# Kernel optimization log

Measured on AMD Instinct MI355X. Metric: run time of the kernel, lower is better.

Reference implementation:

```python
import jax, jax.numpy as jnp
import numpy as np

EPS = 1e-8  # torch F.cosine_similarity default eps


def setup_inputs() -> dict:
    key = jax.random.key(0)
    k1, k2, k3 = jax.random.split(key, 3)
    B, D, C = 65536, 512, 10000
    embeddings = jax.random.normal(k1, (B, D), dtype=jnp.float32)
    labels = jax.random.randint(k2, (B,), 0, C, dtype=jnp.int64)
    prototypes = jax.random.normal(k3, (C, D), dtype=jnp.float32)
    return {"embeddings": embeddings, "labels": labels, "prototypes": prototypes}


def reference(embeddings, labels, prototypes):
    # Batched gather of per-sample prototypes: [B, D]
    protos = prototypes[labels]
    # Cosine similarity per sample (torch eps semantics: clamp norm at eps)
    e_norm = jnp.maximum(jnp.linalg.norm(embeddings, axis=-1), EPS)
    p_norm = jnp.maximum(jnp.linalg.norm(protos, axis=-1), EPS)
    cos = jnp.sum(embeddings * protos, axis=-1) / (e_norm * p_norm)
    return 1.0 - jnp.mean(cos)
```

## Files before the change

kernel.cpp:

```cpp
#include <hip/hip_runtime.h>
#include <math.h>

#define COS_EPS 1e-8f

__global__ __launch_bounds__(256) void assignment_loss_kernel(
    const float* __restrict__ emb,
    const int*   __restrict__ labels,
    const float* __restrict__ protos,
    float*       __restrict__ acc,
    int B, int D)
{
    const int lane           = threadIdx.x & 63;
    const int wave_in_block  = threadIdx.x >> 6;
    const int waves_per_blk  = blockDim.x >> 6;
    const int global_wave    = blockIdx.x * waves_per_blk + wave_in_block;
    const int n_waves        = gridDim.x * waves_per_blk;
    const int nchunks        = D >> 8;

    float local = 0.0f;

    for (int s = global_wave; s < B; s += n_waves) {
        const int lbl = labels[s];
        const float4* __restrict__ e =
            (const float4*)(emb + (size_t)s * (size_t)D);
        const float4* __restrict__ p =
            (const float4*)(protos + (size_t)lbl * (size_t)D);

        float dot = 0.0f, esq = 0.0f, psq = 0.0f;
        #pragma unroll
        for (int c = 0; c < 2; ++c) {
            if (c < nchunks) {
                float4 ev = e[c * 64 + lane];
                float4 pv = p[c * 64 + lane];
                dot = fmaf(ev.x, pv.x, fmaf(ev.y, pv.y, fmaf(ev.z, pv.z, fmaf(ev.w, pv.w, dot))));
                esq = fmaf(ev.x, ev.x, fmaf(ev.y, ev.y, fmaf(ev.z, ev.z, fmaf(ev.w, ev.w, esq))));
                psq = fmaf(pv.x, pv.x, fmaf(pv.y, pv.y, fmaf(pv.z, pv.z, fmaf(pv.w, pv.w, psq))));
            }
        }
        for (int c = 2; c < nchunks; ++c) {
            float4 ev = e[c * 64 + lane];
            float4 pv = p[c * 64 + lane];
            dot = fmaf(ev.x, pv.x, fmaf(ev.y, pv.y, fmaf(ev.z, pv.z, fmaf(ev.w, pv.w, dot))));
            esq = fmaf(ev.x, ev.x, fmaf(ev.y, ev.y, fmaf(ev.z, ev.z, fmaf(ev.w, ev.w, esq))));
            psq = fmaf(pv.x, pv.x, fmaf(pv.y, pv.y, fmaf(pv.z, pv.z, fmaf(pv.w, pv.w, psq))));
        }

        #pragma unroll
        for (int off = 32; off > 0; off >>= 1) {
            dot += __shfl_xor(dot, off, 64);
            esq += __shfl_xor(esq, off, 64);
            psq += __shfl_xor(psq, off, 64);
        }

        if (lane == 0) {
            float en = fmaxf(sqrtf(esq), COS_EPS);
            float pn = fmaxf(sqrtf(psq), COS_EPS);
            local += dot / (en * pn);
        }
    }

    __shared__ float smem[8];
    if (lane == 0) smem[wave_in_block] = local;
    __syncthreads();
    if (threadIdx.x == 0) {
        float bs = 0.0f;
        for (int w = 0; w < waves_per_blk; ++w) bs += smem[w];
        atomicAdd(acc, bs);
    }
}

__global__ void assignment_loss_finalize(const float* __restrict__ acc,
                                         float* __restrict__ out,
                                         float invB)
{
    out[0] = 1.0f - acc[0] * invB;
}

extern "C" void kernel_launch(void* const* d_in, const int* in_sizes, int n_in,
                              void* d_out, int out_size, void* d_ws, size_t ws_size,
                              hipStream_t stream) {
    const float* emb    = (const float*)d_in[0];
    const int*   labels = (const int*)  d_in[1];
    const float* protos = (const float*)d_in[2];
    float*       out    = (float*)d_out;
    float*       acc    = (float*)d_ws;

    const int B = in_sizes[1];
    const int D = in_sizes[0] / B;

    hipMemsetAsync(acc, 0, sizeof(float), stream);

    const int block = 256;
    const int grid  = 1024;
    assignment_loss_kernel<<<grid, block, 0, stream>>>(emb, labels, protos, acc, B, D);
    assignment_loss_finalize<<<1, 1, 0, stream>>>(acc, out, 1.0f / (float)B);
}
```

Measured before the change: 215.2 us.

## Process two samples per wave with nontemporal loads and fuse finalize via ticket

Each wave now handles two samples per iteration, which doubles the loads in flight to hide gather latency. Embedding reads use nontemporal loads so streaming data does not evict cached prototypes. The separate finalize kernel is replaced by a last-block-done ticket reduction over per-block partials. The grid is doubled to 2048 blocks. This adds register pressure and a threadfence/atomic handshake at the end of the kernel.

```diff
diff --git a/kernel.cpp b/kernel.cpp
--- a/kernel.cpp
+++ b/kernel.cpp
@@ -3,77 +3,120 @@
 
 #define COS_EPS 1e-8f
 
+typedef float vfloat4 __attribute__((ext_vector_type(4)));
+
 __global__ __launch_bounds__(256) void assignment_loss_kernel(
     const float* __restrict__ emb,
     const int*   __restrict__ labels,
     const float* __restrict__ protos,
-    float*       __restrict__ acc,
-    int B, int D)
+    float*        __restrict__ partials,
+    unsigned int* __restrict__ ticket,
+    float*        __restrict__ out,
+    int B, int D, float invB)
 {
-    const int lane           = threadIdx.x & 63;
-    const int wave_in_block  = threadIdx.x >> 6;
-    const int waves_per_blk  = blockDim.x >> 6;
-    const int global_wave    = blockIdx.x * waves_per_blk + wave_in_block;
-    const int n_waves        = gridDim.x * waves_per_blk;
-    const int nchunks        = D >> 8;
+    const int lane          = threadIdx.x & 63;
+    const int wave_in_block = threadIdx.x >> 6;
+    const int waves_per_blk = blockDim.x >> 6;
+    const int global_wave   = blockIdx.x * waves_per_blk + wave_in_block;
+    const int n_waves       = gridDim.x * waves_per_blk;
+    const int nchunks       = D >> 8;
 
     float local = 0.0f;
 
-    for (int s = global_wave; s < B; s += n_waves) {
-        const int lbl = labels[s];
-        const float4* __restrict__ e =
-            (const float4*)(emb + (size_t)s * (size_t)D);
-        const float4* __restrict__ p =
-            (const float4*)(protos + (size_t)lbl * (size_t)D);
+    for (int s0 = global_wave; s0 < B; s0 += 2 * n_waves) {
+        const int s1    = s0 + n_waves;
+        const bool has1 = (s1 < B);
 
-        float dot = 0.0f, esq = 0.0f, psq = 0.0f;
+        const int l0 = labels[s0];
+        const int l1 = has1 ? labels[s1] : 0;
+
+        const vfloat4* __restrict__ e0 = (const vfloat4*)(emb    + (size_t)s0 * (size_t)D);
+        const vfloat4* __restrict__ p0 = (const vfloat4*)(protos + (size_t)l0 * (size_t)D);
+        const vfloat4* __restrict__ e1 = (const vfloat4*)(emb    + (size_t)(has1 ? s1 : s0) * (size_t)D);
+        const vfloat4* __restrict__ p1 = (const vfloat4*)(protos + (size_t)l1 * (size_t)D);
+
+        float dot0 = 0.f, esq0 = 0.f, psq0 = 0.f;
+        float dot1 = 0.f, esq1 = 0.f, psq1 = 0.f;
+
         #pragma unroll
         for (int c = 0; c < 2; ++c) {
             if (c < nchunks) {
-                float4 ev = e[c * 64 + lane];
-                float4 pv = p[c * 64 + lane];
-                dot = fmaf(ev.x, pv.x, fmaf(ev.y, pv.y, fmaf(ev.z, pv.z, fmaf(ev.w, pv.w, dot))));
-                esq = fmaf(ev.x, ev.x, fmaf(ev.y, ev.y, fmaf(ev.z, ev.z, fmaf(ev.w, ev.w, esq))));
-                psq = fmaf(pv.x, pv.x, fmaf(pv.y, pv.y, fmaf(pv.z, pv.z, fmaf(pv.w, pv.w, psq))));
+                vfloat4 ev0 = __builtin_nontemporal_load(&e0[c * 64 + lane]);
+                vfloat4 pv0 = p0[c * 64 + lane];
+                vfloat4 ev1 = __builtin_nontemporal_load(&e1[c * 64 + lane]);
+                vfloat4 pv1 = p1[c * 64 + lane];
+
+                dot0 = fmaf(ev0.x, pv0.x, fmaf(ev0.y, pv0.y, fmaf(ev0.z, pv0.z, fmaf(ev0.w, pv0.w, dot0))));
+                esq0 = fmaf(ev0.x, ev0.x, fmaf(ev0.y, ev0.y, fmaf(ev0.z, ev0.z, fmaf(ev0.w, ev0.w, esq0))));
+                psq0 = fmaf(pv0.x, pv0.x, fmaf(pv0.y, pv0.y, fmaf(pv0.z, pv0.z, fmaf(pv0.w, pv0.w, psq0))));
+                dot1 = fmaf(ev1.x, pv1.x, fmaf(ev1.y, pv1.y, fmaf(ev1.z, pv1.z, fmaf(ev1.w, pv1.w, dot1))));
+                esq1 = fmaf(ev1.x, ev1.x, fmaf(ev1.y, ev1.y, fmaf(ev1.z, ev1.z, fmaf(ev1.w, ev1.w, esq1))));
+                psq1 = fmaf(pv1.x, pv1.x, fmaf(pv1.y, pv1.y, fmaf(pv1.z, pv1.z, fmaf(pv1.w, pv1.w, psq1))));
             }
         }
         for (int c = 2; c < nchunks; ++c) {
-            float4 ev = e[c * 64 + lane];
-            float4 pv = p[c * 64 + lane];
-            dot = fmaf(ev.x, pv.x, fmaf(ev.y, pv.y, fmaf(ev.z, pv.z, fmaf(ev.w, pv.w, dot))));
-            esq = fmaf(ev.x, ev.x, fmaf(ev.y, ev.y, fmaf(ev.z, ev.z, fmaf(ev.w, ev.w, esq))));
-            psq = fmaf(pv.x, pv.x, fmaf(pv.y, pv.y, fmaf(pv.z, pv.z, fmaf(pv.w, pv.w, psq))));
+            vfloat4 ev0 = __builtin_nontemporal_load(&e0[c * 64 + lane]);
+            vfloat4 pv0 = p0[c * 64 + lane];
+            vfloat4 ev1 = __builtin_nontemporal_load(&e1[c * 64 + lane]);
+            vfloat4 pv1 = p1[c * 64 + lane];
+            dot0 = fmaf(ev0.x, pv0.x, fmaf(ev0.y, pv0.y, fmaf(ev0.z, pv0.z, fmaf(ev0.w, pv0.w, dot0))));
+            esq0 = fmaf(ev0.x, ev0.x, fmaf(ev0.y, ev0.y, fmaf(ev0.z, ev0.z, fmaf(ev0.w, ev0.w, esq0))));
+            psq0 = fmaf(pv0.x, pv0.x, fmaf(pv0.y, pv0.y, fmaf(pv0.z, pv0.z, fmaf(pv0.w, pv0.w, psq0))));
+            dot1 = fmaf(ev1.x, pv1.x, fmaf(ev1.y, pv1.y, fmaf(ev1.z, pv1.z, fmaf(ev1.w, pv1.w, dot1))));
+            esq1 = fmaf(ev1.x, ev1.x, fmaf(ev1.y, ev1.y, fmaf(ev1.z, ev1.z, fmaf(ev1.w, ev1.w, esq1))));
+            psq1 = fmaf(pv1.x, pv1.x, fmaf(pv1.y, pv1.y, fmaf(pv1.z, pv1.z, fmaf(pv1.w, pv1.w, psq1))));
         }
 
         #pragma unroll
         for (int off = 32; off > 0; off >>= 1) {
-            dot += __shfl_xor(dot, off, 64);
-            esq += __shfl_xor(esq, off, 64);
-            psq += __shfl_xor(psq, off, 64);
+            dot0 += __shfl_xor(dot0, off, 64);
+            esq0 += __shfl_xor(esq0, off, 64);
+            psq0 += __shfl_xor(psq0, off, 64);
+            dot1 += __shfl_xor(dot1, off, 64);
+            esq1 += __shfl_xor(esq1, off, 64);
+            psq1 += __shfl_xor(psq1, off, 64);
         }
 
         if (lane == 0) {
-            float en = fmaxf(sqrtf(esq), COS_EPS);
-            float pn = fmaxf(sqrtf(psq), COS_EPS);
-            local += dot / (en * pn);
+            float en0 = fmaxf(sqrtf(esq0), COS_EPS);
+            float pn0 = fmaxf(sqrtf(psq0), COS_EPS);
+            local += dot0 / (en0 * pn0);
+            if (has1) {
+                float en1 = fmaxf(sqrtf(esq1), COS_EPS);
+                float pn1 = fmaxf(sqrtf(psq1), COS_EPS);
+                local += dot1 / (en1 * pn1);
+            }
         }
     }
 
     __shared__ float smem[8];
+    __shared__ bool  am_last;
     if (lane == 0) smem[wave_in_block] = local;
     __syncthreads();
     if (threadIdx.x == 0) {
         float bs = 0.0f;
         for (int w = 0; w < waves_per_blk; ++w) bs += smem[w];
-        atomicAdd(acc, bs);
+        partials[blockIdx.x] = bs;
+        __threadfence();
+        unsigned t = atomicAdd(ticket, 1u);
+        am_last = (t == (unsigned)gridDim.x - 1u);
     }
-}
+    __syncthreads();
 
-__global__ void assignment_loss_finalize(const float* __restrict__ acc,
-                                         float* __restrict__ out,
-                                         float invB)
-{
-    out[0] = 1.0f - acc[0] * invB;
+    if (am_last) {
+        __threadfence();
+        float s = 0.0f;
+        for (int i = threadIdx.x; i < gridDim.x; i += blockDim.x) s += partials[i];
+        #pragma unroll
+        for (int off = 32; off > 0; off >>= 1) s += __shfl_xor(s, off, 64);
+        if (lane == 0) smem[wave_in_block] = s;
+        __syncthreads();
+        if (threadIdx.x == 0) {
+            float total = 0.0f;
+            for (int w = 0; w < waves_per_blk; ++w) total += smem[w];
+            out[0] = 1.0f - total * invB;
+        }
+    }
 }
 
 extern "C" void kernel_launch(void* const* d_in, const int* in_sizes, int n_in,
@@ -83,15 +126,17 @@
     const int*   labels = (const int*)  d_in[1];
     const float* protos = (const float*)d_in[2];
     float*       out    = (float*)d_out;
-    float*       acc    = (float*)d_ws;
+
+    unsigned int* ticket   = (unsigned int*)d_ws;
+    float*        partials = (float*)((char*)d_ws + 256);
 
     const int B = in_sizes[1];
     const int D = in_sizes[0] / B;
 
-    hipMemsetAsync(acc, 0, sizeof(float), stream);
+    hipMemsetAsync(ticket, 0, sizeof(unsigned int), stream);
 
     const int block = 256;
-    const int grid  = 1024;
-    assignment_loss_kernel<<<grid, block, 0, stream>>>(emb, labels, protos, acc, B, D);
-    assignment_loss_finalize<<<1, 1, 0, stream>>>(acc, out, 1.0f / (float)B);
+    const int grid  = 2048;
+    assignment_loss_kernel<<<grid, block, 0, stream>>>(
+        emb, labels, protos, partials, ticket, out, B, D, 1.0f / (float)B);
 }
```

Measured after the change: 298.3 us. +38.6%, slower.

## Precompute inverse row norms and defer wave reductions in weighted dot pass

Applied to the files above, without the earlier changes.

Splits the loss into two kernels. The first computes inverse L2 norms for every embedding row and every prototype row into workspace. The second computes only per-sample dot products scaled by the precomputed inverse norms, processing four samples per wave iteration for memory-level parallelism. It reduces across lanes once at the end instead of running three shuffle reductions per sample. The cost is a second full read of the embeddings plus one extra kernel launch, in exchange for much less per-sample shuffle and divide latency.

```diff
diff --git a/kernel.cpp b/kernel.cpp
--- a/kernel.cpp
+++ b/kernel.cpp
@@ -3,68 +3,123 @@
 
 #define COS_EPS 1e-8f
 
-__global__ __launch_bounds__(256) void assignment_loss_kernel(
+typedef float vfloat4 __attribute__((ext_vector_type(4)));
+
+__device__ __forceinline__ float dot4(vfloat4 a, vfloat4 b) {
+    return fmaf(a.x, b.x, fmaf(a.y, b.y, fmaf(a.z, b.z, a.w * b.w)));
+}
+
+__global__ __launch_bounds__(256) void row_inv_norm_kernel(
+    const float* __restrict__ emb,
+    const float* __restrict__ protos,
+    float* __restrict__ inv_en,
+    float* __restrict__ inv_pn,
+    int B, int C, int D)
+{
+    const int lane = threadIdx.x & 63;
+    const int gw   = (blockIdx.x * blockDim.x + threadIdx.x) >> 6;
+    const int nw   = (gridDim.x * blockDim.x) >> 6;
+    const int nchunks = D >> 8;
+    const int R = B + C;
+
+    for (int r = gw; r < R; r += nw) {
+        const float* row = (r < B) ? (emb + (size_t)r * (size_t)D)
+                                   : (protos + (size_t)(r - B) * (size_t)D);
+        const vfloat4* v = (const vfloat4*)row;
+        float ssq = 0.0f;
+        if (nchunks == 2) {
+            vfloat4 a = v[lane];
+            vfloat4 b = v[64 + lane];
+            ssq = dot4(a, a) + dot4(b, b);
+        } else {
+            for (int c = 0; c < nchunks; ++c) {
+                vfloat4 a = v[c * 64 + lane];
+                ssq += dot4(a, a);
+            }
+        }
+        #pragma unroll
+        for (int off = 32; off > 0; off >>= 1) ssq += __shfl_xor(ssq, off, 64);
+        if (lane == 0) {
+            float inv = 1.0f / fmaxf(sqrtf(ssq), COS_EPS);
+            if (r < B) inv_en[r] = inv; else inv_pn[r - B] = inv;
+        }
+    }
+}
+
+__global__ __launch_bounds__(256) void weighted_dot_kernel(
     const float* __restrict__ emb,
     const int*   __restrict__ labels,
     const float* __restrict__ protos,
+    const float* __restrict__ inv_en,
+    const float* __restrict__ inv_pn,
     float*       __restrict__ acc,
     int B, int D)
 {
-    const int lane           = threadIdx.x & 63;
-    const int wave_in_block  = threadIdx.x >> 6;
-    const int waves_per_blk  = blockDim.x >> 6;
-    const int global_wave    = blockIdx.x * waves_per_blk + wave_in_block;
-    const int n_waves        = gridDim.x * waves_per_blk;
-    const int nchunks        = D >> 8;
+    const int lane = threadIdx.x & 63;
+    const int wib  = threadIdx.x >> 6;
+    const int wpb  = blockDim.x >> 6;
+    const int gw   = blockIdx.x * wpb + wib;
+    const int nw   = gridDim.x * wpb;
+    const int nchunks = D >> 8;
 
     float local = 0.0f;
 
-    for (int s = global_wave; s < B; s += n_waves) {
-        const int lbl = labels[s];
-        const float4* __restrict__ e =
-            (const float4*)(emb + (size_t)s * (size_t)D);
-        const float4* __restrict__ p =
-            (const float4*)(protos + (size_t)lbl * (size_t)D);
+    if (nchunks == 2 && (B % (4 * nw)) == 0) {
+        for (int s = gw; s < B; s += 4 * nw) {
+            const int s0 = s, s1 = s + nw, s2 = s + 2 * nw, s3 = s + 3 * nw;
+            const int l0 = labels[s0], l1 = labels[s1], l2 = labels[s2], l3 = labels[s3];
 
-        float dot = 0.0f, esq = 0.0f, psq = 0.0f;
-        #pragma unroll
-        for (int c = 0; c < 2; ++c) {
-            if (c < nchunks) {
-                float4 ev = e[c * 64 + lane];
-                float4 pv = p[c * 64 + lane];
-                dot = fmaf(ev.x, pv.x, fmaf(ev.y, pv.y, fmaf(ev.z, pv.z, fmaf(ev.w, pv.w, dot))));
-                esq = fmaf(ev.x, ev.x, fmaf(ev.y, ev.y, fmaf(ev.z, ev.z, fmaf(ev.w, ev.w, esq))));
-                psq = fmaf(pv.x, pv.x, fmaf(pv.y, pv.y, fmaf(pv.z, pv.z, fmaf(pv.w, pv.w, psq))));
-            }
+            const vfloat4* e0 = (const vfloat4*)(emb    + (size_t)s0 * (size_t)D);
+            const vfloat4* e1 = (const vfloat4*)(emb    + (size_t)s1 * (size_t)D);
+            const vfloat4* e2 = (const vfloat4*)(emb    + (size_t)s2 * (size_t)D);
+            const vfloat4* e3 = (const vfloat4*)(emb    + (size_t)s3 * (size_t)D);
+            const vfloat4* p0 = (const vfloat4*)(protos + (size_t)l0 * (size_t)D);
+            const vfloat4* p1 = (const vfloat4*)(protos + (size_t)l1 * (size_t)D);
+            const vfloat4* p2 = (const vfloat4*)(protos + (size_t)l2 * (size_t)D);
+            const vfloat4* p3 = (const vfloat4*)(protos + (size_t)l3 * (size_t)D);
+
+            vfloat4 ea0 = e0[lane],      eb0 = e0[64 + lane];
+            vfloat4 ea1 = e1[lane],      eb1 = e1[64 + lane];
+            vfloat4 ea2 = e2[lane],      eb2 = e2[64 + lane];
+            vfloat4 ea3 = e3[lane],      eb3 = e3[64 + lane];
+            vfloat4 pa0 = p0[lane],      pb0 = p0[64 + lane];
+            vfloat4 pa1 = p1[lane],      pb1 = p1[64 + lane];
+            vfloat4 pa2 = p2[lane],      pb2 = p2[64 + lane];
+            vfloat4 pa3 = p3[lane],      pb3 = p3[64 + lane];
+
+            const float w0 = inv_en[s0] * inv_pn[l0];
+            const float w1 = inv_en[s1] * inv_pn[l1];
+            const float w2 = inv_en[s2] * inv_pn[l2];
+            const float w3 = inv_en[s3] * inv_pn[l3];
+
+            const float pd0 = dot4(ea0, pa0) + dot4(eb0, pb0);
+            const float pd1 = dot4(ea1, pa1) + dot4(eb1, pb1);
+            const float pd2 = dot4(ea2, pa2) + dot4(eb2, pb2);
+            const float pd3 = dot4(ea3, pa3) + dot4(eb3, pb3);
+
+            local = fmaf(pd0, w0, fmaf(pd1, w1, fmaf(pd2, w2, fmaf(pd3, w3, local))));
         }
-        for (int c = 2; c < nchunks; ++c) {
-            float4 ev = e[c * 64 + lane];
-            float4 pv = p[c * 64 + lane];
-            dot = fmaf(ev.x, pv.x, fmaf(ev.y, pv.y, fmaf(ev.z, pv.z, fmaf(ev.w, pv.w, dot))));
-            esq = fmaf(ev.x, ev.x, fmaf(ev.y, ev.y, fmaf(ev.z, ev.z, fmaf(ev.w, ev.w, esq))));
-            psq = fmaf(pv.x, pv.x, fmaf(pv.y, pv.y, fmaf(pv.z, pv.z, fmaf(pv.w, pv.w, psq))));
-        }
-
-        #pragma unroll
-        for (int off = 32; off > 0; off >>= 1) {
-            dot += __shfl_xor(dot, off, 64);
-            esq += __shfl_xor(esq, off, 64);
-            psq += __shfl_xor(psq, off, 64);
-        }
-
-        if (lane == 0) {
-            float en = fmaxf(sqrtf(esq), COS_EPS);
-            float pn = fmaxf(sqrtf(psq), COS_EPS);
-            local += dot / (en * pn);
+    } else {
+        for (int s = gw; s < B; s += nw) {
+            const int l = labels[s];
+            const vfloat4* e = (const vfloat4*)(emb    + (size_t)s * (size_t)D);
+            const vfloat4* p = (const vfloat4*)(protos + (size_t)l * (size_t)D);
+            float pd = 0.0f;
+            for (int c = 0; c < nchunks; ++c)
+                pd += dot4(e[c * 64 + lane], p[c * 64 + lane]);
+            local = fmaf(pd, inv_en[s] * inv_pn[l], local);
         }
     }
 
+    #pragma unroll
+    for (int off = 32; off > 0; off >>= 1) local += __shfl_xor(local, off, 64);
+
     __shared__ float smem[8];
-    if (lane == 0) smem[wave_in_block] = local;
+    if (lane == 0) smem[wib] = local;
     __syncthreads();
     if (threadIdx.x == 0) {
         float bs = 0.0f;
-        for (int w = 0; w < waves_per_blk; ++w) bs += smem[w];
+        for (int w = 0; w < wpb; ++w) bs += smem[w];
         atomicAdd(acc, bs);
     }
 }
@@ -83,15 +138,18 @@
     const int*   labels = (const int*)  d_in[1];
     const float* protos = (const float*)d_in[2];
     float*       out    = (float*)d_out;
-    float*       acc    = (float*)d_ws;
 
     const int B = in_sizes[1];
     const int D = in_sizes[0] / B;
+    const int C = in_sizes[2] / D;
+
+    float* acc    = (float*)d_ws;
+    float* inv_en = (float*)((char*)d_ws + 256);
+    float* inv_pn = inv_en + B;
 
     hipMemsetAsync(acc, 0, sizeof(float), stream);
 
-    const int block = 256;
-    const int grid  = 1024;
-    assignment_loss_kernel<<<grid, block, 0, stream>>>(emb, labels, protos, acc, B, D);
+    row_inv_norm_kernel<<<2048, 256, 0, stream>>>(emb, protos, inv_en, inv_pn, B, C, D);
+    weighted_dot_kernel<<<1024, 256, 0, stream>>>(emb, labels, protos, inv_en, inv_pn, acc, B, D);
     assignment_loss_finalize<<<1, 1, 0, stream>>>(acc, out, 1.0f / (float)B);
 }
```

After: 245.1 us. 1.14x slower.

## Process four samples per wave with 16-lane groups and prefetch labels

Applied to the files above, without the earlier changes.

Specializes the D=512 case so each wave handles four samples at once, with 16 lanes per sample each issuing eight float4 loads for the embedding and the prototype up front. The next sample's label is prefetched one iteration ahead, and the cross-lane reduction is shortened to four shuffle steps within each 16-lane group. This is meant to raise memory-level parallelism and hide the dependent label-then-prototype gather latency in a bandwidth-bound kernel. It costs more registers per thread, and it falls back to the old path when D or B do not fit the assumptions.

```diff
diff --git a/kernel.cpp b/kernel.cpp
--- a/kernel.cpp
+++ b/kernel.cpp
@@ -2,6 +2,12 @@
 #include <math.h>
 
 #define COS_EPS 1e-8f
+
+typedef float vfloat4 __attribute__((ext_vector_type(4)));
+
+__device__ __forceinline__ float dot4(vfloat4 a, vfloat4 b) {
+    return fmaf(a.x, b.x, fmaf(a.y, b.y, fmaf(a.z, b.z, a.w * b.w)));
+}
 
 __global__ __launch_bounds__(256) void assignment_loss_kernel(
     const float* __restrict__ emb,
@@ -10,61 +16,94 @@
     float*       __restrict__ acc,
     int B, int D)
 {
-    const int lane           = threadIdx.x & 63;
-    const int wave_in_block  = threadIdx.x >> 6;
-    const int waves_per_blk  = blockDim.x >> 6;
-    const int global_wave    = blockIdx.x * waves_per_blk + wave_in_block;
-    const int n_waves        = gridDim.x * waves_per_blk;
-    const int nchunks        = D >> 8;
+    const int lane = threadIdx.x & 63;
+    const int grp  = lane >> 4;
+    const int gl   = lane & 15;
+    const int wib  = threadIdx.x >> 6;
+    const int wpb  = blockDim.x >> 6;
+    const int gw   = blockIdx.x * wpb + wib;
+    const int nw   = gridDim.x * wpb;
 
     float local = 0.0f;
 
-    for (int s = global_wave; s < B; s += n_waves) {
-        const int lbl = labels[s];
-        const float4* __restrict__ e =
-            (const float4*)(emb + (size_t)s * (size_t)D);
-        const float4* __restrict__ p =
-            (const float4*)(protos + (size_t)lbl * (size_t)D);
+    if (D == 512 && (B % (4 * nw)) == 0) {
+        const int iters = B / (4 * nw);
+        int s   = gw * 4 + grp;
+        int lbl = labels[s];
 
-        float dot = 0.0f, esq = 0.0f, psq = 0.0f;
-        #pragma unroll
-        for (int c = 0; c < 2; ++c) {
-            if (c < nchunks) {
-                float4 ev = e[c * 64 + lane];
-                float4 pv = p[c * 64 + lane];
-                dot = fmaf(ev.x, pv.x, fmaf(ev.y, pv.y, fmaf(ev.z, pv.z, fmaf(ev.w, pv.w, dot))));
-                esq = fmaf(ev.x, ev.x, fmaf(ev.y, ev.y, fmaf(ev.z, ev.z, fmaf(ev.w, ev.w, esq))));
-                psq = fmaf(pv.x, pv.x, fmaf(pv.y, pv.y, fmaf(pv.z, pv.z, fmaf(pv.w, pv.w, psq))));
+        for (int i = 0; i < iters; ++i) {
+            const int s_next   = s + 4 * nw;
+            const int lbl_next = (i + 1 < iters) ? labels[s_next] : 0;
+
+            const vfloat4* e = (const vfloat4*)(emb    + (size_t)s   * 512);
+            const vfloat4* p = (const vfloat4*)(protos + (size_t)lbl * 512);
+
+            vfloat4 ev[8], pv[8];
+            #pragma unroll
+            for (int c = 0; c < 8; ++c) ev[c] = e[c * 16 + gl];
+            #pragma unroll
+            for (int c = 0; c < 8; ++c) pv[c] = p[c * 16 + gl];
+
+            float dot = 0.f, esq = 0.f, psq = 0.f;
+            #pragma unroll
+            for (int c = 0; c < 8; ++c) {
+                dot += dot4(ev[c], pv[c]);
+                esq += dot4(ev[c], ev[c]);
+                psq += dot4(pv[c], pv[c]);
             }
+
+            #pragma unroll
+            for (int off = 8; off > 0; off >>= 1) {
+                dot += __shfl_xor(dot, off, 64);
+                esq += __shfl_xor(esq, off, 64);
+                psq += __shfl_xor(psq, off, 64);
+            }
+
+            if (gl == 0) {
+                float en = fmaxf(sqrtf(esq), COS_EPS);
+                float pn = fmaxf(sqrtf(psq), COS_EPS);
+                local += dot / (en * pn);
+            }
+
+            s = s_next; lbl = lbl_next;
         }
-        for (int c = 2; c < nchunks; ++c) {
-            float4 ev = e[c * 64 + lane];
-            float4 pv = p[c * 64 + lane];
-            dot = fmaf(ev.x, pv.x, fmaf(ev.y, pv.y, fmaf(ev.z, pv.z, fmaf(ev.w, pv.w, dot))));
-            esq = fmaf(ev.x, ev.x, fmaf(ev.y, ev.y, fmaf(ev.z, ev.z, fmaf(ev.w, ev.w, esq))));
-            psq = fmaf(pv.x, pv.x, fmaf(pv.y, pv.y, fmaf(pv.z, pv.z, fmaf(pv.w, pv.w, psq))));
-        }
-
-        #pragma unroll
-        for (int off = 32; off > 0; off >>= 1) {
-            dot += __shfl_xor(dot, off, 64);
-            esq += __shfl_xor(esq, off, 64);
-            psq += __shfl_xor(psq, off, 64);
-        }
-
-        if (lane == 0) {
-            float en = fmaxf(sqrtf(esq), COS_EPS);
-            float pn = fmaxf(sqrtf(psq), COS_EPS);
-            local += dot / (en * pn);
+    } else {
+        const int nchunks = D >> 8;
+        for (int smp = gw; smp < B; smp += nw) {
+            const int l = labels[smp];
+            const vfloat4* e = (const vfloat4*)(emb    + (size_t)smp * (size_t)D);
+            const vfloat4* p = (const vfloat4*)(protos + (size_t)l   * (size_t)D);
+            float dot = 0.f, esq = 0.f, psq = 0.f;
+            for (int c = 0; c < nchunks; ++c) {
+                vfloat4 ev = e[c * 64 + lane];
+                vfloat4 pv = p[c * 64 + lane];
+                dot += dot4(ev, pv);
+                esq += dot4(ev, ev);
+                psq += dot4(pv, pv);
+            }
+            #pragma unroll
+            for (int off = 32; off > 0; off >>= 1) {
+                dot += __shfl_xor(dot, off, 64);
+                esq += __shfl_xor(esq, off, 64);
+                psq += __shfl_xor(psq, off, 64);
+            }
+            if (lane == 0) {
+                float en = fmaxf(sqrtf(esq), COS_EPS);
+                float pn = fmaxf(sqrtf(psq), COS_EPS);
+                local += dot / (en * pn);
+            }
         }
     }
 
+    #pragma unroll
+    for (int off = 32; off > 0; off >>= 1) local += __shfl_xor(local, off, 64);
+
     __shared__ float smem[8];
-    if (lane == 0) smem[wave_in_block] = local;
+    if (lane == 0) smem[wib] = local;
     __syncthreads();
     if (threadIdx.x == 0) {
         float bs = 0.0f;
-        for (int w = 0; w < waves_per_blk; ++w) bs += smem[w];
+        for (int w = 0; w < wpb; ++w) bs += smem[w];
         atomicAdd(acc, bs);
     }
 }
```

After: 209.2 us. 2.8% less time.
